# Kernel tuning notes

Hardware: AMD Instinct MI355X
Metric: run time of the kernel (lower is better)

Reference implementation:

```python
import jax, jax.numpy as jnp
import numpy as np

B, N, H, A = 2048, 49, 1024, 512


def setup_inputs() -> dict:
    key = jax.random.key(0)
    ks = jax.random.split(key, 9)
    s_h = 1.0 / np.sqrt(H)
    s_a = 1.0 / np.sqrt(A)
    return {
        "hidden": jax.random.normal(ks[0], (B, H), jnp.float32),
        "img_features": jax.random.normal(ks[1], (B, N, H), jnp.float32),
        "coverage": jax.random.uniform(ks[2], (B, N), jnp.float32),
        "W_h": jax.random.uniform(ks[3], (H, A), jnp.float32, -s_h, s_h),
        "b_h": jax.random.uniform(ks[4], (A,), jnp.float32, -s_h, s_h),
        "W_img": jax.random.uniform(ks[5], (H, A), jnp.float32, -s_h, s_h),
        "b_img": jax.random.uniform(ks[6], (A,), jnp.float32, -s_h, s_h),
        "W_cov": jax.random.uniform(ks[7], (1, A), jnp.float32, -1.0, 1.0),
        "v": jax.random.uniform(ks[8], (A,), jnp.float32, -s_a, s_a),
    }


def reference(hidden, img_features, coverage, W_h, b_h, W_img, b_img, W_cov, v):
    # h_proj: (B, 1, A); img_proj: (B, N, A)
    h_proj = (hidden @ W_h + b_h)[:, None, :]
    img_proj = jnp.einsum("bnh,ha->bna", img_features, W_img) + b_img
    # coverage projection: (B, N, 1) @ (1, A) -> (B, N, A)
    cov_proj = coverage[:, :, None] * W_cov[0]
    energy = jnp.tanh(h_proj + img_proj + cov_proj)
    scores = jnp.einsum("bna,a->bn", energy, v)  # (B, N)
    alpha = jax.nn.softmax(scores, axis=1)
    context = jnp.einsum("bn,bnh->bh", alpha, img_features)
    return (context, alpha)
```

## Files before the change

### kernel.cpp

```cpp
#include <hip/hip_runtime.h>
#include <cstdint>
#include <cstddef>

#define B_ 2048
#define N_ 49
#define H_ 1024
#define A_ 512
#define M_ (B_*N_)

typedef __attribute__((ext_vector_type(8))) short short8;
typedef __attribute__((ext_vector_type(8))) unsigned short ushort8;
typedef __attribute__((ext_vector_type(4))) float f32x4;
typedef unsigned int u32;

__device__ inline unsigned short f2bf(float f){
  union { float f; unsigned u; } v; v.f = f;
  unsigned r = v.u + 0x7FFFu + ((v.u >> 16) & 1u);
  return (unsigned short)(r >> 16);
}
__device__ inline float bf2f(unsigned short h){
  union { u32 u; float f; } v; v.u = ((u32)h) << 16; return v.f;
}
__device__ inline float fast_tanh(float x){
  float e = __expf(2.0f*x);
  return 1.0f - 2.0f/(e + 1.0f);
}
__device__ inline void gl16(const void* g, void* l){
  __builtin_amdgcn_global_load_lds((const __attribute__((address_space(1))) u32*)g,
                                   (__attribute__((address_space(3))) u32*)l, 16, 0, 0);
}

__global__ __launch_bounds__(256) void k_transpose(
    const float* __restrict__ Wh, const float* __restrict__ Wimg,
    unsigned short* __restrict__ WtH, unsigned short* __restrict__ WtImg){
  const float* src = blockIdx.y ? Wimg : Wh;
  unsigned short* dst = blockIdx.y ? WtImg : WtH;
  int tk = (blockIdx.x & 31) * 32;
  int ta = (blockIdx.x >> 5) * 32;
  __shared__ unsigned short tile[32][33];
  int t = threadIdx.x;
  int r = t >> 3, c4 = t & 7;
  float4 vv = *(const float4*)(src + (size_t)(tk + r)*A_ + ta + c4*4);
  tile[c4*4+0][r] = f2bf(vv.x);
  tile[c4*4+1][r] = f2bf(vv.y);
  tile[c4*4+2][r] = f2bf(vv.z);
  tile[c4*4+3][r] = f2bf(vv.w);
  __syncthreads();
  ushort4 o;
  o.x = tile[r][c4*4+0]; o.y = tile[r][c4*4+1];
  o.z = tile[r][c4*4+2]; o.w = tile[r][c4*4+3];
  *(ushort4*)(dst + (size_t)(ta + r)*H_ + tk + c4*4) = o;
}

__global__ __launch_bounds__(256) void k_convert(
    const float* __restrict__ src, unsigned short* __restrict__ dst, size_t n8){
  size_t i = (size_t)blockIdx.x*256 + threadIdx.x;
  size_t stride = (size_t)gridDim.x*256;
  const float4* s4 = (const float4*)src;
  ushort8* d8 = (ushort8*)dst;
  for (; i < n8; i += stride){
    float4 a = s4[2*i], b = s4[2*i+1];
    ushort8 o;
    o[0]=f2bf(a.x); o[1]=f2bf(a.y); o[2]=f2bf(a.z); o[3]=f2bf(a.w);
    o[4]=f2bf(b.x); o[5]=f2bf(b.y); o[6]=f2bf(b.z); o[7]=f2bf(b.w);
    d8[i] = o;
  }
}

#define BK 64
#define LDK 72

__device__ inline void gemm_tile(const float* __restrict__ Asrc,
                                 const unsigned short* __restrict__ Wt,
                                 int m0, int a0, f32x4 acc[4][4],
                                 unsigned short (*sA)[LDK], unsigned short (*sB)[LDK]){
  const int t = threadIdx.x;
  const int l = t & 63, w = t >> 6;
  const int wr = w >> 1, wc = w & 1;
  const int g = l >> 4, c = l & 15;
  #pragma unroll
  for (int m=0;m<4;m++)
    #pragma unroll
    for (int n=0;n<4;n++)
      acc[m][n] = f32x4{0.f,0.f,0.f,0.f};

  for (int k0 = 0; k0 < H_; k0 += BK){
    #pragma unroll
    for (int i=0;i<8;i++){
      int f = i*256 + t;
      int row = f >> 4, c4 = f & 15;
      float4 vv = *(const float4*)(Asrc + (size_t)(m0+row)*H_ + k0 + c4*4);
      ushort4 h; h.x=f2bf(vv.x); h.y=f2bf(vv.y); h.z=f2bf(vv.z); h.w=f2bf(vv.w);
      *(ushort4*)&sA[row][c4*4] = h;
    }
    #pragma unroll
    for (int i=0;i<8;i++){
      int f = i*256 + t;
      int row = f >> 4, c4 = f & 15;
      *(ushort4*)&sB[row][c4*4] = *(const ushort4*)(Wt + (size_t)(a0+row)*H_ + k0 + c4*4);
    }
    __syncthreads();
    #pragma unroll
    for (int kk=0; kk<BK; kk+=32){
      short8 aF[4], bF[4];
      #pragma unroll
      for (int m=0;m<4;m++) aF[m] = *(const short8*)&sA[wr*64 + m*16 + c][kk + g*8];
      #pragma unroll
      for (int n=0;n<4;n++) bF[n] = *(const short8*)&sB[wc*64 + n*16 + c][kk + g*8];
      #pragma unroll
      for (int m=0;m<4;m++)
        #pragma unroll
        for (int n=0;n<4;n++)
          acc[m][n] = __builtin_amdgcn_mfma_f32_16x16x32_bf16(aF[m], bF[n], acc[m][n], 0, 0, 0);
    }
    __syncthreads();
  }
}

__global__ __launch_bounds__(256) void k_hproj(
    const float* __restrict__ hidden, const unsigned short* __restrict__ WtH,
    const float* __restrict__ b_h, float* __restrict__ hproj){
  __shared__ __align__(16) unsigned short sA[128][LDK];
  __shared__ __align__(16) unsigned short sB[128][LDK];
  f32x4 acc[4][4];
  int m0 = blockIdx.x * 128, a0 = blockIdx.y * 128;
  gemm_tile(hidden, WtH, m0, a0, acc, sA, sB);
  const int l = threadIdx.x & 63, w = threadIdx.x >> 6;
  const int wr = w >> 1, wc = w & 1, g = l >> 4, c = l & 15;
  #pragma unroll
  for (int n=0;n<4;n++){
    int col = a0 + wc*64 + n*16 + c;
    float bh = b_h[col];
    #pragma unroll
    for (int m=0;m<4;m++)
      #pragma unroll
      for (int r=0;r<4;r++){
        int rowg = m0 + wr*64 + m*16 + g*4 + r;
        hproj[(size_t)rowg*A_ + col] = acc[m][n][r] + bh;
      }
  }
}

__global__ __launch_bounds__(256) void k_scores_b(
    const unsigned short* __restrict__ Ab, const unsigned short* __restrict__ Wt,
    const float* __restrict__ hproj, const float* __restrict__ b_img,
    const float* __restrict__ cov, const float* __restrict__ Wcov,
    const float* __restrict__ v, float* __restrict__ scoresP){
  __shared__ __align__(16) unsigned short sA[128][64];
  __shared__ __align__(16) unsigned short sB[128][64];
  __shared__ float sH[4][128];
  __shared__ float sS[128];
  const int t = threadIdx.x;
  const int l = t & 63, w = t >> 6;
  const int wr = w >> 1, wc = w & 1;
  const int g = l >> 4, c = l & 15;

  const int nwg = (M_/128)*(A_/128);
  int bid = blockIdx.x;
  int wg = (bid & 7) * (nwg/8) + (bid >> 3);
  int m0 = (wg >> 2) * 128;
  int a0 = (wg & 3) * 128;

  const int srow = w*32 + (l >> 3);
  const int scol = (l & 7) * 8;
  const unsigned short* gA = Ab + (size_t)(m0 + srow)*H_ + scol;
  const unsigned short* gB = Wt + (size_t)(a0 + srow)*H_ + scol;
  char* lA = (char*)sA + w*4096;
  char* lB = (char*)sB + w*4096;

  f32x4 acc[4][4];
  #pragma unroll
  for (int m=0;m<4;m++)
    #pragma unroll
    for (int n=0;n<4;n++)
      acc[m][n] = f32x4{0.f,0.f,0.f,0.f};

  for (int k0 = 0; k0 < H_; k0 += 64){
    #pragma unroll
    for (int cc=0; cc<4; cc++){
      gl16(gA + (size_t)cc*8*H_ + k0, lA + cc*1024);
      gl16(gB + (size_t)cc*8*H_ + k0, lB + cc*1024);
    }
    __syncthreads();
    #pragma unroll
    for (int kk=0; kk<64; kk+=32){
      short8 aF[4], bF[4];
      #pragma unroll
      for (int m=0;m<4;m++) aF[m] = *(const short8*)&sA[wr*64 + m*16 + c][kk + g*8];
      #pragma unroll
      for (int n=0;n<4;n++) bF[n] = *(const short8*)&sB[wc*64 + n*16 + c][kk + g*8];
      #pragma unroll
      for (int m=0;m<4;m++)
        #pragma unroll
        for (int n=0;n<4;n++)
          acc[m][n] = __builtin_amdgcn_mfma_f32_16x16x32_bf16(aF[m], bF[n], acc[m][n], 0, 0, 0);
    }
    __syncthreads();
  }

  int bFirst = m0 / N_;
  int bLast  = (m0 + 127) / N_;
  int nB = bLast - bFirst + 1;
  if (t < 128) sS[t] = 0.f;
  for (int idx = t; idx < nB*128; idx += 256){
    int bb = idx >> 7, a = idx & 127;
    sH[bb][a] = hproj[(size_t)(bFirst + bb)*A_ + a0 + a];
  }
  __syncthreads();

  float vv[4], bi[4], wcv[4];
  #pragma unroll
  for (int n=0;n<4;n++){
    int col = a0 + wc*64 + n*16 + c;
    vv[n] = v[col]; bi[n] = b_img[col]; wcv[n] = Wcov[col];
  }
  #pragma unroll
  for (int m=0;m<4;m++)
    #pragma unroll
    for (int r=0;r<4;r++){
      int rowl = wr*64 + m*16 + g*4 + r;
      int rowg = m0 + rowl;
      int bb = rowg / N_;
      float cv = cov[rowg];
      float s = 0.f;
      #pragma unroll
      for (int n=0;n<4;n++){
        float x = acc[m][n][r] + sH[bb - bFirst][wc*64 + n*16 + c] + bi[n] + cv*wcv[n];
        s += fast_tanh(x) * vv[n];
      }
      s += __shfl_xor(s, 1, 16);
      s += __shfl_xor(s, 2, 16);
      s += __shfl_xor(s, 4, 16);
      s += __shfl_xor(s, 8, 16);
      if (c == 0) atomicAdd(&sS[rowl], s);
    }
  __syncthreads();
  if (t < 128) scoresP[(size_t)(a0 >> 7)*M_ + m0 + t] = sS[t];
}

__global__ __launch_bounds__(256) void k_scores_f(
    const float* __restrict__ img, const unsigned short* __restrict__ WtImg,
    const float* __restrict__ hproj, const float* __restrict__ b_img,
    const float* __restrict__ cov, const float* __restrict__ Wcov,
    const float* __restrict__ v, float* __restrict__ scores){
  __shared__ __align__(16) unsigned short sA[128][LDK];
  __shared__ __align__(16) unsigned short sB[128][LDK];
  __shared__ float sH[4][128];
  f32x4 acc[4][4];
  int m0 = blockIdx.x * 128, a0 = blockIdx.y * 128;
  gemm_tile(img, WtImg, m0, a0, acc, sA, sB);
  int bFirst = m0 / N_;
  int bLast  = (m0 + 127) / N_;
  int nB = bLast - bFirst + 1;
  for (int idx = threadIdx.x; idx < nB*128; idx += 256){
    int bb = idx >> 7, a = idx & 127;
    sH[bb][a] = hproj[(size_t)(bFirst + bb)*A_ + a0 + a];
  }
  __syncthreads();
  const int l = threadIdx.x & 63, w = threadIdx.x >> 6;
  const int wr = w >> 1, wc = w & 1, g = l >> 4, c = l & 15;
  float vv[4], bi[4], wcv[4];
  #pragma unroll
  for (int n=0;n<4;n++){
    int col = a0 + wc*64 + n*16 + c;
    vv[n] = v[col]; bi[n] = b_img[col]; wcv[n] = Wcov[col];
  }
  #pragma unroll
  for (int m=0;m<4;m++)
    #pragma unroll
    for (int r=0;r<4;r++){
      int rowg = m0 + wr*64 + m*16 + g*4 + r;
      int bb = rowg / N_;
      float cv = cov[rowg];
      float s = 0.f;
      #pragma unroll
      for (int n=0;n<4;n++){
        float x = acc[m][n][r] + sH[bb - bFirst][wc*64 + n*16 + c] + bi[n] + cv*wcv[n];
        s += fast_tanh(x) * vv[n];
      }
      s += __shfl_xor(s, 1, 16);
      s += __shfl_xor(s, 2, 16);
      s += __shfl_xor(s, 4, 16);
      s += __shfl_xor(s, 8, 16);
      if (c == 0) atomicAdd(&scores[rowg], s);
    }
}

__global__ __launch_bounds__(256) void k_ctx_b(
    const unsigned short* __restrict__ imgb, const float* __restrict__ scoresP,
    float* __restrict__ outCtx, float* __restrict__ outAlpha){
  int b = blockIdx.x;
  __shared__ float sAl[N_];
  int t = threadIdx.x;
  if (t < 64){
    float s = -1e30f;
    if (t < N_){
      size_t rg = (size_t)b*N_ + t;
      s = scoresP[rg] + scoresP[M_ + rg] + scoresP[2*(size_t)M_ + rg] + scoresP[3*(size_t)M_ + rg];
    }
    float m = s;
    #pragma unroll
    for (int off=32; off>=1; off>>=1) m = fmaxf(m, __shfl_xor(m, off));
    float e = (t < N_) ? __expf(s - m) : 0.f;
    float sum = e;
    #pragma unroll
    for (int off=32; off>=1; off>>=1) sum += __shfl_xor(sum, off);
    float al = e / sum;
    if (t < N_){ sAl[t] = al; outAlpha[(size_t)b*N_ + t] = al; }
  }
  __syncthreads();
  float4 acc = {0.f,0.f,0.f,0.f};
  #pragma unroll 7
  for (int n=0;n<N_;n++){
    float al = sAl[n];
    ushort4 x = *(const ushort4*)(imgb + ((size_t)b*N_ + n)*H_ + t*4);
    acc.x += al*bf2f(x.x); acc.y += al*bf2f(x.y);
    acc.z += al*bf2f(x.z); acc.w += al*bf2f(x.w);
  }
  *(float4*)(outCtx + (size_t)b*H_ + t*4) = acc;
}

__global__ __launch_bounds__(256) void k_ctx_f(
    const float* __restrict__ img, const float* __restrict__ scores,
    float* __restrict__ outCtx, float* __restrict__ outAlpha){
  int b = blockIdx.x;
  __shared__ float sAl[N_];
  int t = threadIdx.x;
  if (t < 64){
    float s = (t < N_) ? scores[(size_t)b*N_ + t] : -1e30f;
    float m = s;
    #pragma unroll
    for (int off=32; off>=1; off>>=1) m = fmaxf(m, __shfl_xor(m, off));
    float e = (t < N_) ? __expf(s - m) : 0.f;
    float sum = e;
    #pragma unroll
    for (int off=32; off>=1; off>>=1) sum += __shfl_xor(sum, off);
    float al = e / sum;
    if (t < N_){ sAl[t] = al; outAlpha[(size_t)b*N_ + t] = al; }
  }
  __syncthreads();
  const float4* ib = (const float4*)(img + (size_t)b*N_*H_);
  float4 acc = {0.f,0.f,0.f,0.f};
  for (int n=0;n<N_;n++){
    float al = sAl[n];
    float4 x = ib[n*(H_/4) + t];
    acc.x += al*x.x; acc.y += al*x.y; acc.z += al*x.z; acc.w += al*x.w;
  }
  *(float4*)(outCtx + (size_t)b*H_ + t*4) = acc;
}

extern "C" void kernel_launch(void* const* d_in, const int* in_sizes, int n_in,
                              void* d_out, int out_size, void* d_ws, size_t ws_size,
                              hipStream_t stream){
  const float* hidden = (const float*)d_in[0];
  const float* img    = (const float*)d_in[1];
  const float* cov    = (const float*)d_in[2];
  const float* W_h    = (const float*)d_in[3];
  const float* b_h    = (const float*)d_in[4];
  const float* W_img  = (const float*)d_in[5];
  const float* b_img  = (const float*)d_in[6];
  const float* W_cov  = (const float*)d_in[7];
  const float* v      = (const float*)d_in[8];

  char* ws = (char*)d_ws;
  unsigned short* WtH   = (unsigned short*)ws;
  unsigned short* WtImg = (unsigned short*)(ws + (1u<<20));
  float* hproj   = (float*)(ws + (2u<<20));
  float* scoresP = (float*)(ws + (6u<<20));
  unsigned short* imgb = (unsigned short*)(ws + (8u<<20));

  float* outCtx   = (float*)d_out;
  float* outAlpha = outCtx + (size_t)B_*H_;

  const size_t needed = (8ull<<20) + (size_t)M_*H_*2;

  k_transpose<<<dim3(512, 2), 256, 0, stream>>>(W_h, W_img, WtH, WtImg);
  k_hproj<<<dim3(B_/128, A_/128), 256, 0, stream>>>(hidden, WtH, b_h, hproj);

  if (ws_size >= needed){
    k_convert<<<2048, 256, 0, stream>>>(img, imgb, (size_t)M_*H_/8);
    k_scores_b<<<(M_/128)*(A_/128), 256, 0, stream>>>(imgb, WtImg, hproj, b_img, cov, W_cov, v, scoresP);
    k_ctx_b<<<B_, 256, 0, stream>>>(imgb, scoresP, outCtx, outAlpha);
  } else {
    hipMemsetAsync(scoresP, 0, (size_t)M_*sizeof(float), stream);
    k_scores_f<<<dim3(M_/128, A_/128), 256, 0, stream>>>(img, WtImg, hproj, b_img, cov, W_cov, v, scoresP);
    k_ctx_f<<<B_, 256, 0, stream>>>(img, scoresP, outCtx, outAlpha);
  }
}
```

Baseline: 414.1 us.

## Enlarge scores GEMM tile to 256x256 with double-buffered swizzled LDS pipeline

The fused score GEMM moves from 128x128 tiles with 4 waves to 256x256 tiles with 8 waves. LDS is double-buffered so the next K-slice loads while the current one is multiplied, and an XOR swizzle on the LDS layout avoids bank conflicts. Wave priority is raised around the MFMA bursts. Score partials drop from four A-slices to two, which halves the partial-sum reads in the context kernel, at the cost of 128KB of LDS per block, which limits occupancy.

```diff
diff --git a/kernel.cpp b/kernel.cpp
--- a/kernel.cpp
+++ b/kernel.cpp
@@ -141,91 +141,113 @@
   }
 }
 
-__global__ __launch_bounds__(256) void k_scores_b(
+__global__ __launch_bounds__(512, 2) void k_scores_b8(
     const unsigned short* __restrict__ Ab, const unsigned short* __restrict__ Wt,
     const float* __restrict__ hproj, const float* __restrict__ b_img,
     const float* __restrict__ cov, const float* __restrict__ Wcov,
     const float* __restrict__ v, float* __restrict__ scoresP){
-  __shared__ __align__(16) unsigned short sA[128][64];
-  __shared__ __align__(16) unsigned short sB[128][64];
-  __shared__ float sH[4][128];
-  __shared__ float sS[128];
+  __shared__ __align__(16) char lds[131072];
   const int t = threadIdx.x;
   const int l = t & 63, w = t >> 6;
-  const int wr = w >> 1, wc = w & 1;
+  const int wr = w >> 2, wc = w & 3;
   const int g = l >> 4, c = l & 15;
-
-  const int nwg = (M_/128)*(A_/128);
+  const int cm = (c & 7) << 4;
+
+  const int nwg = (M_/256)*(A_/256);
   int bid = blockIdx.x;
-  int wg = (bid & 7) * (nwg/8) + (bid >> 3);
-  int m0 = (wg >> 2) * 128;
-  int a0 = (wg & 3) * 128;
-
-  const int srow = w*32 + (l >> 3);
-  const int scol = (l & 7) * 8;
-  const unsigned short* gA = Ab + (size_t)(m0 + srow)*H_ + scol;
-  const unsigned short* gB = Wt + (size_t)(a0 + srow)*H_ + scol;
-  char* lA = (char*)sA + w*4096;
-  char* lB = (char*)sB + w*4096;
-
-  f32x4 acc[4][4];
-  #pragma unroll
-  for (int m=0;m<4;m++)
-    #pragma unroll
-    for (int n=0;n<4;n++)
-      acc[m][n] = f32x4{0.f,0.f,0.f,0.f};
-
-  for (int k0 = 0; k0 < H_; k0 += 64){
-    #pragma unroll
-    for (int cc=0; cc<4; cc++){
-      gl16(gA + (size_t)cc*8*H_ + k0, lA + cc*1024);
-      gl16(gB + (size_t)cc*8*H_ + k0, lB + cc*1024);
-    }
-    __syncthreads();
-    #pragma unroll
-    for (int kk=0; kk<64; kk+=32){
+  int wg = (bid & 7)*(nwg/8) + (bid >> 3);
+  const int m0 = (wg >> 1) * 256;
+  const int a0 = (wg & 1) * 256;
+
+  const int rsub = l >> 3;
+  const int ksw  = ((l & 7) ^ rsub) * 8;
+
+  f32x4 acc[8][4] = {};
+
+  auto stage = [&](int bn, int k0){
+    #pragma unroll
+    for (int h=0; h<2; h++){
+      #pragma unroll
+      for (int q=0; q<2; q++){
+        int dA = bn*65536 + h*16384 + w*2048 + q*1024;
+        const unsigned short* ga = Ab + (size_t)(m0 + h*128 + w*16 + q*8 + rsub)*H_ + k0 + ksw;
+        const unsigned short* gb = Wt + (size_t)(a0 + h*128 + w*16 + q*8 + rsub)*H_ + k0 + ksw;
+        gl16(ga, lds + dA);
+        gl16(gb, lds + dA + 32768);
+      }
+    }
+  };
+
+  const int abase = wr*16384;
+  const int bbase = 32768 + (wc>>1)*16384;
+  const int brow  = (wc&1)*64;
+
+  stage(0, 0);
+  for (int tt=0; tt<16; tt++){
+    const int cur = (tt & 1) << 16;
+    if (tt < 15){
+      stage((tt+1)&1, (tt+1)*64);
+      asm volatile("s_waitcnt vmcnt(8)" ::: "memory");
+    } else {
+      asm volatile("s_waitcnt vmcnt(0)" ::: "memory");
+    }
+    asm volatile("s_barrier" ::: "memory");
+    #pragma unroll
+    for (int p=0; p<4; p++){
+      const int mh  = p >> 1;
+      const int kb  = (p & 1) * 64;
       short8 aF[4], bF[4];
       #pragma unroll
-      for (int m=0;m<4;m++) aF[m] = *(const short8*)&sA[wr*64 + m*16 + c][kk + g*8];
-      #pragma unroll
-      for (int n=0;n<4;n++) bF[n] = *(const short8*)&sB[wc*64 + n*16 + c][kk + g*8];
-      #pragma unroll
-      for (int m=0;m<4;m++)
+      for (int i=0;i<4;i++){
+        int rl = (mh*4+i)*16 + c;
+        aF[i] = *(const short8*)(lds + cur + abase + rl*128 + ((kb + g*16) ^ cm));
+      }
+      #pragma unroll
+      for (int n=0;n<4;n++){
+        int rb = brow + n*16 + c;
+        bF[n] = *(const short8*)(lds + cur + bbase + rb*128 + ((kb + g*16) ^ cm));
+      }
+      asm volatile("s_barrier" ::: "memory");
+      __builtin_amdgcn_s_setprio(1);
+      #pragma unroll
+      for (int i=0;i<4;i++)
         #pragma unroll
         for (int n=0;n<4;n++)
-          acc[m][n] = __builtin_amdgcn_mfma_f32_16x16x32_bf16(aF[m], bF[n], acc[m][n], 0, 0, 0);
-    }
-    __syncthreads();
-  }
-
-  int bFirst = m0 / N_;
-  int bLast  = (m0 + 127) / N_;
-  int nB = bLast - bFirst + 1;
-  if (t < 128) sS[t] = 0.f;
-  for (int idx = t; idx < nB*128; idx += 256){
-    int bb = idx >> 7, a = idx & 127;
-    sH[bb][a] = hproj[(size_t)(bFirst + bb)*A_ + a0 + a];
+          acc[mh*4+i][n] = __builtin_amdgcn_mfma_f32_16x16x32_bf16(aF[i], bF[n], acc[mh*4+i][n], 0, 0, 0);
+      __builtin_amdgcn_s_setprio(0);
+      asm volatile("s_barrier" ::: "memory");
+    }
+  }
+
+  float* sS = (float*)lds;
+  float* sH = (float*)lds + 256;
+  const int bFirst = m0 / N_;
+  const int nB = (m0 + 255)/N_ - bFirst + 1;
+  if (t < 256) sS[t] = 0.f;
+  for (int idx = t; idx < nB*256; idx += 512){
+    int bb = idx >> 8, a = idx & 255;
+    sH[bb*256 + a] = hproj[(size_t)(bFirst + bb)*A_ + a0 + a];
   }
   __syncthreads();
 
   float vv[4], bi[4], wcv[4];
   #pragma unroll
   for (int n=0;n<4;n++){
-    int col = a0 + wc*64 + n*16 + c;
-    vv[n] = v[col]; bi[n] = b_img[col]; wcv[n] = Wcov[col];
-  }
-  #pragma unroll
-  for (int m=0;m<4;m++)
+    int colg = a0 + wc*64 + n*16 + c;
+    vv[n] = v[colg]; bi[n] = b_img[colg]; wcv[n] = Wcov[colg];
+  }
+  #pragma unroll
+  for (int m=0;m<8;m++){
     #pragma unroll
     for (int r=0;r<4;r++){
-      int rowl = wr*64 + m*16 + g*4 + r;
+      int rowl = wr*128 + m*16 + g*4 + r;
       int rowg = m0 + rowl;
-      int bb = rowg / N_;
+      int bb = rowg / N_ - bFirst;
       float cv = cov[rowg];
       float s = 0.f;
       #pragma unroll
       for (int n=0;n<4;n++){
-        float x = acc[m][n][r] + sH[bb - bFirst][wc*64 + n*16 + c] + bi[n] + cv*wcv[n];
+        float x = acc[m][n][r] + sH[bb*256 + wc*64 + n*16 + c] + bi[n] + cv*wcv[n];
         s += fast_tanh(x) * vv[n];
       }
       s += __shfl_xor(s, 1, 16);
@@ -234,8 +256,9 @@
       s += __shfl_xor(s, 8, 16);
       if (c == 0) atomicAdd(&sS[rowl], s);
     }
-  __syncthreads();
-  if (t < 128) scoresP[(size_t)(a0 >> 7)*M_ + m0 + t] = sS[t];
+  }
+  __syncthreads();
+  if (t < 256) scoresP[(size_t)(a0 >> 8)*M_ + m0 + t] = sS[t];
 }
 
 __global__ __launch_bounds__(256) void k_scores_f(
@@ -296,7 +319,7 @@
     float s = -1e30f;
     if (t < N_){
       size_t rg = (size_t)b*N_ + t;
-      s = scoresP[rg] + scoresP[M_ + rg] + scoresP[2*(size_t)M_ + rg] + scoresP[3*(size_t)M_ + rg];
+      s = scoresP[rg] + scoresP[(size_t)M_ + rg];
     }
     float m = s;
     #pragma unroll
@@ -379,7 +402,7 @@
 
   if (ws_size >= needed){
     k_convert<<<2048, 256, 0, stream>>>(img, imgb, (size_t)M_*H_/8);
-    k_scores_b<<<(M_/128)*(A_/128), 256, 0, stream>>>(imgb, WtImg, hproj, b_img, cov, W_cov, v, scoresP);
+    k_scores_b8<<<(M_/256)*(A_/256), 512, 0, stream>>>(imgb, WtImg, hproj, b_img, cov, W_cov, v, scoresP);
     k_ctx_b<<<B_, 256, 0, stream>>>(imgb, scoresP, outCtx, outAlpha);
   } else {
     hipMemsetAsync(scoresP, 0, (size_t)M_*sizeof(float), stream);
```

New measurement: 381.9 us. 1.08x faster.
